# Kernel tuning notes

Measured on AMD Instinct MI355X. Metric: run time of the kernel, lower is better.

## Reference

```python
import jax, jax.numpy as jnp
import numpy as np

B, C, D_IN, D_H, D_OUT = 131072, 16, 256, 1024, 256


def setup_inputs() -> dict:
    key = jax.random.key(0)
    k = jax.random.split(key, 6)
    return {
        "x": jax.random.normal(k[0], (B, D_IN), dtype=jnp.float32),
        "cat_ids": jax.random.randint(k[1], (B,), 0, C, dtype=jnp.int32),
        "W1": jax.random.normal(k[2], (C, D_IN, D_H), dtype=jnp.float32) * (1.0 / np.sqrt(D_IN)),
        "b1": jax.random.normal(k[3], (C, D_H), dtype=jnp.float32) * 0.02,
        "W2": jax.random.normal(k[4], (C, D_H, D_OUT), dtype=jnp.float32) * (1.0 / np.sqrt(D_H)),
        "b2": jax.random.normal(k[5], (C, D_OUT), dtype=jnp.float32) * 0.02,
    }


def _routed_linear(x, cat_ids, W, b):
    # Category-routed linear: out[i] = x[i] @ W[cat_ids[i]] + b[cat_ids[i]].
    # Loop over the small fixed category count (not over tokens); each branch
    # is a dense GEMM masked by the routing assignment. This is equivalent to
    # the original gather -> per-category Linear -> scatter/argsort pattern
    # without materializing per-token weight gathers.
    num_categories = W.shape[0]
    out = jnp.zeros((x.shape[0], W.shape[2]), dtype=x.dtype)
    for c in range(num_categories):
        mask = (cat_ids == c)[:, None]
        out = out + jnp.where(mask, x @ W[c] + b[c], jnp.zeros((), x.dtype))
    return out


def reference(x, cat_ids, W1, b1, W2, b2):
    hidden = jax.nn.relu(_routed_linear(x, cat_ids, W1, b1))
    return _routed_linear(hidden, cat_ids, W2, b2)
```

## Files before the change

kernel.cpp:

```cpp
#include <hip/hip_runtime.h>
#include <hip/hip_bf16.h>

#define BB   131072
#define CC   16
#define DIN  256
#define DH   1024
#define DOUT 256
#define TM   64
#define NHB  32
#define NB   512

typedef __attribute__((ext_vector_type(8))) short bf16x8;
typedef __attribute__((ext_vector_type(4))) short short4v;
typedef __attribute__((ext_vector_type(4))) float f32x4;
typedef __attribute__((ext_vector_type(4))) float float4v;

__device__ inline unsigned short f2b(float f) {
  union { float f; unsigned u; } v; v.f = f;
  unsigned u = v.u;
  return (unsigned short)((u + 0x7fffu + ((u >> 16) & 1u)) >> 16);
}

__device__ inline void gload_lds16(const void* g, void* l) {
  __builtin_amdgcn_global_load_lds(
      (const __attribute__((address_space(1))) void*)g,
      (__attribute__((address_space(3))) void*)l, 16, 0, 0);
}

#define MFMA16(a, b, c) __builtin_amdgcn_mfma_f32_16x16x32_bf16((a), (b), (c), 0, 0, 0)

__global__ void hist_k(const int* __restrict__ cat, int* __restrict__ blockhist) {
  __shared__ int h[CC];
  const int tid = threadIdx.x;
  if (tid < CC) h[tid] = 0;
  __syncthreads();
  const int i = blockIdx.x * 256 + tid;
  atomicAdd(&h[cat[i]], 1);
  __syncthreads();
  if (tid < CC) blockhist[blockIdx.x * CC + tid] = h[tid];
}

__global__ void offsets2_k(const int* __restrict__ blockhist,
                           int* __restrict__ counts, int* __restrict__ padoff,
                           int* __restrict__ base) {
  __shared__ int part[CC][64];
  __shared__ int pref[CC][64];
  __shared__ int scnt[CC];
  __shared__ int spad[CC + 1];
  const int tid = threadIdx.x;
  const int c = tid >> 6;
  const int g = tid & 63;
  int h[8];
  int s = 0;
#pragma unroll
  for (int i = 0; i < 8; i++) {
    h[i] = blockhist[(g * 8 + i) * CC + c];
    s += h[i];
  }
  part[c][g] = s;
  __syncthreads();
  if (g == 0) {
    int r = 0;
    for (int j = 0; j < 64; j++) { pref[c][j] = r; r += part[c][j]; }
    scnt[c] = r;
  }
  __syncthreads();
  if (tid == 0) {
    int acc = 0;
    for (int c2 = 0; c2 < CC; c2++) {
      spad[c2] = acc;
      padoff[c2] = acc;
      counts[c2] = scnt[c2];
      acc += ((scnt[c2] + TM - 1) / TM) * TM;
    }
    spad[CC] = acc;
    padoff[CC] = acc;
  }
  __syncthreads();
  int run = spad[c] + pref[c][g];
#pragma unroll
  for (int i = 0; i < 8; i++) {
    base[(g * 8 + i) * CC + c] = run;
    run += h[i];
  }
}

__global__ void scatter2_k(const int* __restrict__ cat, const int* __restrict__ base,
                           int* __restrict__ idx) {
  __shared__ int cur[CC];
  const int tid = threadIdx.x;
  if (tid < CC) cur[tid] = base[blockIdx.x * CC + tid];
  __syncthreads();
  const int i = blockIdx.x * 256 + tid;
  const int c = cat[i];
  const int pos = atomicAdd(&cur[c], 1);
  idx[pos] = i;
}

__global__ void conv_w1_k(const float* __restrict__ W1, short* __restrict__ w1b) {
  int t = blockIdx.x * blockDim.x + threadIdx.x;
  int n  = t & 1023;
  int j8 = (t >> 10) & 31;
  int c  = t >> 15;
  const float* src = W1 + (size_t)c * DIN * DH;
  bf16x8 o;
#pragma unroll
  for (int i = 0; i < 8; i++)
    o[i] = (short)f2b(src[(size_t)(j8 * 8 + i) * DH + n]);
  char* dst = (char*)w1b + (size_t)c * 524288
            + (n >> 5) * 16384 + ((n >> 4) & 1) * 8192 + (j8 >> 2) * 1024
            + ((n & 15) + 16 * (j8 & 3)) * 16;
  *(bf16x8*)dst = o;
}

__global__ void conv_w2_k(const float* __restrict__ W2, short* __restrict__ w2b) {
  int t = blockIdx.x * blockDim.x + threadIdx.x;
  int n  = t & 255;
  int j8 = (t >> 8) & 127;
  int c  = t >> 15;
  const float* src = W2 + (size_t)c * DH * DOUT;
  bf16x8 o;
#pragma unroll
  for (int i = 0; i < 8; i++)
    o[i] = (short)f2b(src[(size_t)(j8 * 8 + i) * DOUT + n]);
  char* dst = (char*)w2b + (size_t)c * 524288
            + (j8 >> 2) * 16384 + (n >> 4) * 1024
            + ((n & 15) + 16 * (j8 & 3)) * 16;
  *(bf16x8*)dst = o;
}

#define W2OFF  32768
#define HSOFF  65536
#define TKOFF  69632
#define B1OFF  69888
#define B2OFF  73984
#define SMSZ   75008

__launch_bounds__(512, 4)
__global__ void mlp_k(const float* __restrict__ x,
                      const float* __restrict__ b1,
                      const float* __restrict__ b2,
                      const short* __restrict__ w1b,
                      const short* __restrict__ w2b,
                      const int* __restrict__ idx,
                      const int* __restrict__ padoff,
                      const int* __restrict__ counts,
                      float* __restrict__ out) {
  __shared__ __align__(16) char sm[SMSZ];

  const int bhw = blockIdx.x;
  const int wg = (bhw & 7) * 258 + (bhw >> 3);
  const int p = wg * TM;
  const int total = padoff[CC];
  if (p >= total) return;
  int c = 0;
  while (padoff[c + 1] <= p) c++;
  const int cnt = counts[c];
  const int start = p - padoff[c];

  const int tid  = threadIdx.x;
  const int lane = tid & 63;
  const int w    = tid >> 6;
  const int wt   = w >> 1;
  const int wh   = w & 1;
  const int lrow = lane & 15;
  const int lgrp = lane >> 4;

  char*  hsb   = sm + HSOFF;
  int*   toksp = (int*)(sm + TKOFF);
  float* b1s   = (float*)(sm + B1OFF);
  float* b2s   = (float*)(sm + B2OFF);

  {
    const int r = tid >> 3;
    const int q = tid & 7;
    const int pos = start + r;
    int tok = (pos < cnt) ? idx[p + r] : -1;
    if (q == 0) toksp[r] = tok;
    char* tilebase = sm + ((r >> 4) * 8 + q) * 1024 + (r & 15) * 16;
    if (tok >= 0) {
      const float4v* src = (const float4v*)(x + (size_t)tok * DIN) + q * 8;
#pragma unroll
      for (int m = 0; m < 4; m++) {
        float4v v0 = src[2 * m];
        float4v v1 = src[2 * m + 1];
        bf16x8 o;
        o[0] = (short)f2b(v0[0]); o[1] = (short)f2b(v0[1]);
        o[2] = (short)f2b(v0[2]); o[3] = (short)f2b(v0[3]);
        o[4] = (short)f2b(v1[0]); o[5] = (short)f2b(v1[1]);
        o[6] = (short)f2b(v1[2]); o[7] = (short)f2b(v1[3]);
        *(bf16x8*)(tilebase + m * 256) = o;
      }
    } else {
      bf16x8 z = {0, 0, 0, 0, 0, 0, 0, 0};
#pragma unroll
      for (int m = 0; m < 4; m++)
        *(bf16x8*)(tilebase + m * 256) = z;
    }
    if (tid < 256) ((f32x4*)b1s)[tid] = ((const f32x4*)(b1 + (size_t)c * DH))[tid];
    if (tid < 64)  ((f32x4*)b2s)[tid] = ((const f32x4*)(b2 + (size_t)c * DOUT))[tid];
  }
  __syncthreads();

  bf16x8 xf[8];
#pragma unroll
  for (int ks = 0; ks < 8; ks++)
    xf[ks] = *(const bf16x8*)(sm + (wt * 8 + ks) * 1024 + lane * 16);
  __syncthreads();

  const char* w1g = (const char*)w1b + (size_t)c * 524288;
  const char* w2g = (const char*)w2b + (size_t)c * 524288;

  auto stage1 = [&](int i) {
    const char* src = w1g + (size_t)i * 16384;
    char* dst = sm + (i & 1) * 16384;
#pragma unroll
    for (int j = 0; j < 2; j++) {
      int chunk = (w * 2 + j) * 1024;
      gload_lds16(src + chunk + lane * 16, dst + chunk);
    }
  };
  auto stage2 = [&](int i) {
    const char* src = w2g + (size_t)i * 16384;
    char* dst = sm + W2OFF + (i & 1) * 16384;
#pragma unroll
    for (int j = 0; j < 2; j++) {
      int chunk = (w * 2 + j) * 1024;
      gload_lds16(src + chunk + lane * 16, dst + chunk);
    }
  };

  stage1(0);
  stage2(0);
  asm volatile("s_waitcnt vmcnt(0)" ::: "memory");
  __syncthreads();

  f32x4 acc2[8];
#pragma unroll
  for (int ni = 0; ni < 8; ni++)
    acc2[ni] = (f32x4){0.f, 0.f, 0.f, 0.f};

  const int rtok = wt * 16 + lrow;
  char* hswr = hsb + wt * 1024 + (lrow + 16 * (wh * 2 + (lgrp >> 1))) * 16 + (lgrp & 1) * 8;

  for (int hb = 0; hb < NHB; hb++) {
    const char* w1c = sm + (hb & 1) * 16384 + wh * 8192;
    const char* w2c = sm + W2OFF + (hb & 1) * 16384 + wh * 8192;

    if (hb < NHB - 1) { stage1(hb + 1); stage2(hb + 1); }

    f32x4 acc1a = (f32x4){0.f, 0.f, 0.f, 0.f};
    f32x4 acc1b = (f32x4){0.f, 0.f, 0.f, 0.f};
#pragma unroll
    for (int ks = 0; ks < 8; ks += 2) {
      bf16x8 a0 = *(const bf16x8*)(w1c + ks * 1024 + lane * 16);
      bf16x8 a1 = *(const bf16x8*)(w1c + (ks + 1) * 1024 + lane * 16);
      acc1a = MFMA16(a0, xf[ks], acc1a);
      acc1b = MFMA16(a1, xf[ks + 1], acc1b);
    }
    {
      const int n0 = wh * 16 + lgrp * 4;
      f32x4 bv = *(const f32x4*)(b1s + hb * 32 + n0);
      short4v h;
#pragma unroll
      for (int jj = 0; jj < 4; jj++)
        h[jj] = (short)f2b(fmaxf(acc1a[jj] + acc1b[jj] + bv[jj], 0.0f));
      *(short4v*)hswr = h;
    }
    asm volatile("s_waitcnt vmcnt(4) lgkmcnt(0)" ::: "memory");
    __builtin_amdgcn_s_barrier();

    bf16x8 hf = *(const bf16x8*)(hsb + wt * 1024 + lane * 16);
#pragma unroll
    for (int ni = 0; ni < 8; ni++) {
      bf16x8 a2 = *(const bf16x8*)(w2c + ni * 1024 + lane * 16);
      acc2[ni] = MFMA16(a2, hf, acc2[ni]);
    }
    asm volatile("s_waitcnt vmcnt(2) lgkmcnt(0)" ::: "memory");
    __builtin_amdgcn_s_barrier();
  }

  const int tok = toksp[rtok];
  if (tok >= 0) {
#pragma unroll
    for (int ni = 0; ni < 8; ni++) {
      const int n0 = (wh * 8 + ni) * 16 + lgrp * 4;
      f32x4 bv = *(const f32x4*)(b2s + n0);
      f32x4 v = acc2[ni] + bv;
      *(f32x4*)(out + (size_t)tok * DOUT + n0) = v;
    }
  }
}

extern "C" void kernel_launch(void* const* d_in, const int* in_sizes, int n_in,
                              void* d_out, int out_size, void* d_ws, size_t ws_size,
                              hipStream_t stream) {
  (void)in_sizes; (void)n_in; (void)out_size; (void)ws_size;
  const float* x   = (const float*)d_in[0];
  const int*   cat = (const int*)d_in[1];
  const float* W1  = (const float*)d_in[2];
  const float* b1  = (const float*)d_in[3];
  const float* W2  = (const float*)d_in[4];
  const float* b2  = (const float*)d_in[5];
  float* out = (float*)d_out;

  char* ws = (char*)d_ws;
  int* counts    = (int*)(ws);
  int* padoff    = (int*)(ws + 128);
  int* blockhist = (int*)(ws + 4096);
  int* base      = (int*)(ws + 65536);
  int* idx       = (int*)(ws + 131072);
  short* w1b     = (short*)(ws + (1 << 20));
  short* w2b     = (short*)(ws + (1 << 20) + 8388608);

  hist_k<<<NB, 256, 0, stream>>>(cat, blockhist);
  offsets2_k<<<1, 1024, 0, stream>>>(blockhist, counts, padoff, base);
  scatter2_k<<<NB, 256, 0, stream>>>(cat, base, idx);
  conv_w1_k<<<2048, 256, 0, stream>>>(W1, w1b);
  conv_w2_k<<<2048, 256, 0, stream>>>(W2, w2b);

  const int ntiles = BB / TM + CC;
  mlp_k<<<ntiles, 512, 0, stream>>>(x, b1, b2, w1b, w2b, idx, padoff, counts, out);
}
```

Baseline: 236.6 us.

## Warp-specialize MLP kernel into producer/consumer waves with 128-row tiles

```diff
diff --git a/kernel.cpp b/kernel.cpp
--- a/kernel.cpp
+++ b/kernel.cpp
@@ -6,25 +6,18 @@
 #define DIN  256
 #define DH   1024
 #define DOUT 256
-#define TM   64
+#define TM   128
 #define NHB  32
 #define NB   512
 
 typedef __attribute__((ext_vector_type(8))) short bf16x8;
 typedef __attribute__((ext_vector_type(4))) short short4v;
 typedef __attribute__((ext_vector_type(4))) float f32x4;
-typedef __attribute__((ext_vector_type(4))) float float4v;
 
 __device__ inline unsigned short f2b(float f) {
   union { float f; unsigned u; } v; v.f = f;
   unsigned u = v.u;
   return (unsigned short)((u + 0x7fffu + ((u >> 16) & 1u)) >> 16);
-}
-
-__device__ inline void gload_lds16(const void* g, void* l) {
-  __builtin_amdgcn_global_load_lds(
-      (const __attribute__((address_space(1))) void*)g,
-      (__attribute__((address_space(3))) void*)l, 16, 0, 0);
 }
 
 #define MFMA16(a, b, c) __builtin_amdgcn_mfma_f32_16x16x32_bf16((a), (b), (c), 0, 0, 0)
@@ -129,14 +122,13 @@
   *(bf16x8*)dst = o;
 }
 
-#define W2OFF  32768
 #define HSOFF  65536
-#define TKOFF  69632
-#define B1OFF  69888
-#define B2OFF  73984
-#define SMSZ   75008
-
-__launch_bounds__(512, 4)
+#define TKOFF  81920
+#define B1OFF  82432
+#define B2OFF  86528
+#define SMSZ   87552
+
+__launch_bounds__(1024, 4)
 __global__ void mlp_k(const float* __restrict__ x,
                       const float* __restrict__ b1,
                       const float* __restrict__ b2,
@@ -149,7 +141,7 @@
   __shared__ __align__(16) char sm[SMSZ];
 
   const int bhw = blockIdx.x;
-  const int wg = (bhw & 7) * 258 + (bhw >> 3);
+  const int wg = (bhw & 7) * 130 + (bhw >> 3);
   const int p = wg * TM;
   const int total = padoff[CC];
   if (p >= total) return;
@@ -161,12 +153,10 @@
   const int tid  = threadIdx.x;
   const int lane = tid & 63;
   const int w    = tid >> 6;
-  const int wt   = w >> 1;
-  const int wh   = w & 1;
   const int lrow = lane & 15;
   const int lgrp = lane >> 4;
 
-  char*  hsb   = sm + HSOFF;
+  char*  hs0   = sm + HSOFF;
   int*   toksp = (int*)(sm + TKOFF);
   float* b1s   = (float*)(sm + B1OFF);
   float* b2s   = (float*)(sm + B2OFF);
@@ -179,11 +169,11 @@
     if (q == 0) toksp[r] = tok;
     char* tilebase = sm + ((r >> 4) * 8 + q) * 1024 + (r & 15) * 16;
     if (tok >= 0) {
-      const float4v* src = (const float4v*)(x + (size_t)tok * DIN) + q * 8;
+      const f32x4* src = (const f32x4*)(x + (size_t)tok * DIN) + q * 8;
 #pragma unroll
       for (int m = 0; m < 4; m++) {
-        float4v v0 = src[2 * m];
-        float4v v1 = src[2 * m + 1];
+        f32x4 v0 = src[2 * m];
+        f32x4 v1 = src[2 * m + 1];
         bf16x8 o;
         o[0] = (short)f2b(v0[0]); o[1] = (short)f2b(v0[1]);
         o[2] = (short)f2b(v0[2]); o[3] = (short)f2b(v0[3]);
@@ -202,92 +192,94 @@
   }
   __syncthreads();
 
-  bf16x8 xf[8];
-#pragma unroll
-  for (int ks = 0; ks < 8; ks++)
-    xf[ks] = *(const bf16x8*)(sm + (wt * 8 + ks) * 1024 + lane * 16);
-  __syncthreads();
+  const bool isprod = (w < 8);
+  const int tp = w & 3;
+  const int ph = (w >> 2) & 1;
+  const int cw = w & 7;
+  const int tq = cw & 1;
+  const int oq = cw >> 1;
+
+  bf16x8 xf[2][8];
+  if (isprod) {
+#pragma unroll
+    for (int t = 0; t < 2; t++)
+#pragma unroll
+      for (int ks = 0; ks < 8; ks++)
+        xf[t][ks] = *(const bf16x8*)(sm + (size_t)((2 * tp + t) * 8 + ks) * 1024 + lane * 16);
+  }
+
+  f32x4 acc2[4][4];
+  if (!isprod) {
+#pragma unroll
+    for (int j = 0; j < 4; j++)
+#pragma unroll
+      for (int i = 0; i < 4; i++)
+        acc2[j][i] = (f32x4){0.f, 0.f, 0.f, 0.f};
+  }
 
   const char* w1g = (const char*)w1b + (size_t)c * 524288;
   const char* w2g = (const char*)w2b + (size_t)c * 524288;
 
-  auto stage1 = [&](int i) {
-    const char* src = w1g + (size_t)i * 16384;
-    char* dst = sm + (i & 1) * 16384;
-#pragma unroll
-    for (int j = 0; j < 2; j++) {
-      int chunk = (w * 2 + j) * 1024;
-      gload_lds16(src + chunk + lane * 16, dst + chunk);
+  for (int hb = 0; hb <= NHB; hb++) {
+    if (isprod) {
+      if (hb < NHB) {
+        const char* w1p = w1g + hb * 16384 + ph * 8192;
+        f32x4 p0 = (f32x4){0.f, 0.f, 0.f, 0.f};
+        f32x4 p1 = (f32x4){0.f, 0.f, 0.f, 0.f};
+#pragma unroll
+        for (int ks = 0; ks < 8; ks++) {
+          bf16x8 a = *(const bf16x8*)(w1p + ks * 1024 + lane * 16);
+          p0 = MFMA16(a, xf[0][ks], p0);
+          p1 = MFMA16(a, xf[1][ks], p1);
+        }
+        f32x4 bv = *(const f32x4*)(b1s + hb * 32 + ph * 16 + lgrp * 4);
+        char* hw = hs0 + (hb & 1) * 8192
+                 + (lrow + 16 * (ph * 2 + (lgrp >> 1))) * 16 + (lgrp & 1) * 8;
+        short4v h0, h1;
+#pragma unroll
+        for (int jj = 0; jj < 4; jj++) {
+          h0[jj] = (short)f2b(fmaxf(p0[jj] + bv[jj], 0.0f));
+          h1[jj] = (short)f2b(fmaxf(p1[jj] + bv[jj], 0.0f));
+        }
+        *(short4v*)(hw + (2 * tp) * 1024)     = h0;
+        *(short4v*)(hw + (2 * tp + 1) * 1024) = h1;
+      }
+    } else {
+      if (hb > 0) {
+        const char* hr  = hs0 + ((hb - 1) & 1) * 8192;
+        const char* w2p = w2g + (size_t)(hb - 1) * 16384 + oq * 4096;
+        bf16x8 a2[4];
+#pragma unroll
+        for (int j = 0; j < 4; j++)
+          a2[j] = *(const bf16x8*)(w2p + j * 1024 + lane * 16);
+#pragma unroll
+        for (int i = 0; i < 4; i++) {
+          bf16x8 hf = *(const bf16x8*)(hr + (4 * tq + i) * 1024 + lane * 16);
+#pragma unroll
+          for (int j = 0; j < 4; j++)
+            acc2[j][i] = MFMA16(a2[j], hf, acc2[j][i]);
+        }
+      }
     }
-  };
-  auto stage2 = [&](int i) {
-    const char* src = w2g + (size_t)i * 16384;
-    char* dst = sm + W2OFF + (i & 1) * 16384;
-#pragma unroll
-    for (int j = 0; j < 2; j++) {
-      int chunk = (w * 2 + j) * 1024;
-      gload_lds16(src + chunk + lane * 16, dst + chunk);
-    }
-  };
-
-  stage1(0);
-  stage2(0);
-  asm volatile("s_waitcnt vmcnt(0)" ::: "memory");
-  __syncthreads();
-
-  f32x4 acc2[8];
-#pragma unroll
-  for (int ni = 0; ni < 8; ni++)
-    acc2[ni] = (f32x4){0.f, 0.f, 0.f, 0.f};
-
-  const int rtok = wt * 16 + lrow;
-  char* hswr = hsb + wt * 1024 + (lrow + 16 * (wh * 2 + (lgrp >> 1))) * 16 + (lgrp & 1) * 8;
-
-  for (int hb = 0; hb < NHB; hb++) {
-    const char* w1c = sm + (hb & 1) * 16384 + wh * 8192;
-    const char* w2c = sm + W2OFF + (hb & 1) * 16384 + wh * 8192;
-
-    if (hb < NHB - 1) { stage1(hb + 1); stage2(hb + 1); }
-
-    f32x4 acc1a = (f32x4){0.f, 0.f, 0.f, 0.f};
-    f32x4 acc1b = (f32x4){0.f, 0.f, 0.f, 0.f};
-#pragma unroll
-    for (int ks = 0; ks < 8; ks += 2) {
-      bf16x8 a0 = *(const bf16x8*)(w1c + ks * 1024 + lane * 16);
-      bf16x8 a1 = *(const bf16x8*)(w1c + (ks + 1) * 1024 + lane * 16);
-      acc1a = MFMA16(a0, xf[ks], acc1a);
-      acc1b = MFMA16(a1, xf[ks + 1], acc1b);
-    }
-    {
-      const int n0 = wh * 16 + lgrp * 4;
-      f32x4 bv = *(const f32x4*)(b1s + hb * 32 + n0);
-      short4v h;
-#pragma unroll
-      for (int jj = 0; jj < 4; jj++)
-        h[jj] = (short)f2b(fmaxf(acc1a[jj] + acc1b[jj] + bv[jj], 0.0f));
-      *(short4v*)hswr = h;
-    }
-    asm volatile("s_waitcnt vmcnt(4) lgkmcnt(0)" ::: "memory");
+    asm volatile("s_waitcnt lgkmcnt(0)" ::: "memory");
     __builtin_amdgcn_s_barrier();
-
-    bf16x8 hf = *(const bf16x8*)(hsb + wt * 1024 + lane * 16);
-#pragma unroll
-    for (int ni = 0; ni < 8; ni++) {
-      bf16x8 a2 = *(const bf16x8*)(w2c + ni * 1024 + lane * 16);
-      acc2[ni] = MFMA16(a2, hf, acc2[ni]);
-    }
-    asm volatile("s_waitcnt vmcnt(2) lgkmcnt(0)" ::: "memory");
-    __builtin_amdgcn_s_barrier();
-  }
-
-  const int tok = toksp[rtok];
-  if (tok >= 0) {
-#pragma unroll
-    for (int ni = 0; ni < 8; ni++) {
-      const int n0 = (wh * 8 + ni) * 16 + lgrp * 4;
-      f32x4 bv = *(const f32x4*)(b2s + n0);
-      f32x4 v = acc2[ni] + bv;
-      *(f32x4*)(out + (size_t)tok * DOUT + n0) = v;
+    __builtin_amdgcn_sched_barrier(0);
+  }
+
+  if (!isprod) {
+#pragma unroll
+    for (int i = 0; i < 4; i++) {
+      const int rr = (4 * tq + i) * 16 + lrow;
+      const int tok = toksp[rr];
+      if (tok >= 0) {
+#pragma unroll
+        for (int j = 0; j < 4; j++) {
+          const int n0 = (4 * oq + j) * 16 + lgrp * 4;
+          f32x4 bv = *(const f32x4*)(b2s + n0);
+          f32x4 v = acc2[j][i] + bv;
+          *(f32x4*)(out + (size_t)tok * DOUT + n0) = v;
+        }
+      }
     }
   }
 }
@@ -320,5 +312,5 @@
   conv_w2_k<<<2048, 256, 0, stream>>>(W2, w2b);
 
   const int ntiles = BB / TM + CC;
-  mlp_k<<<ntiles, 512, 0, stream>>>(x, b1, b2, w1b, w2b, idx, padoff, counts, out);
-}
+  mlp_k<<<ntiles, 1024, 0, stream>>>(x, b1, b2, w1b, w2b, idx, padoff, counts, out);
+}
```

Result: slower. 641.1 us (+171.0%).

## Double token tile to 128 rows so each wave reuses weight fragments

Applied to the files above, without the earlier changes.

```diff
diff --git a/kernel.cpp b/kernel.cpp
--- a/kernel.cpp
+++ b/kernel.cpp
@@ -6,14 +6,13 @@
 #define DIN  256
 #define DH   1024
 #define DOUT 256
-#define TM   64
-#define NHB  32
+#define TM   128
+#define NHB  16
 #define NB   512
 
 typedef __attribute__((ext_vector_type(8))) short bf16x8;
 typedef __attribute__((ext_vector_type(4))) short short4v;
 typedef __attribute__((ext_vector_type(4))) float f32x4;
-typedef __attribute__((ext_vector_type(4))) float float4v;
 
 __device__ inline unsigned short f2b(float f) {
   union { float f; unsigned u; } v; v.f = f;
@@ -108,7 +107,7 @@
   for (int i = 0; i < 8; i++)
     o[i] = (short)f2b(src[(size_t)(j8 * 8 + i) * DH + n]);
   char* dst = (char*)w1b + (size_t)c * 524288
-            + (n >> 5) * 16384 + ((n >> 4) & 1) * 8192 + (j8 >> 2) * 1024
+            + (n >> 6) * 32768 + ((n >> 4) & 3) * 8192 + (j8 >> 2) * 1024
             + ((n & 15) + 16 * (j8 & 3)) * 16;
   *(bf16x8*)dst = o;
 }
@@ -124,19 +123,19 @@
   for (int i = 0; i < 8; i++)
     o[i] = (short)f2b(src[(size_t)(j8 * 8 + i) * DOUT + n]);
   char* dst = (char*)w2b + (size_t)c * 524288
-            + (j8 >> 2) * 16384 + (n >> 4) * 1024
+            + (j8 >> 3) * 32768 + (n >> 4) * 2048 + ((j8 >> 2) & 1) * 1024
             + ((n & 15) + 16 * (j8 & 3)) * 16;
   *(bf16x8*)dst = o;
 }
 
-#define W2OFF  32768
-#define HSOFF  65536
-#define TKOFF  69632
-#define B1OFF  69888
-#define B2OFF  73984
-#define SMSZ   75008
-
-__launch_bounds__(512, 4)
+#define W2OFF  65536
+#define HSOFF  131072
+#define TKOFF  147456
+#define B1OFF  147968
+#define B2OFF  152064
+#define SMSZ   153088
+
+__launch_bounds__(512, 2)
 __global__ void mlp_k(const float* __restrict__ x,
                       const float* __restrict__ b1,
                       const float* __restrict__ b2,
@@ -149,7 +148,7 @@
   __shared__ __align__(16) char sm[SMSZ];
 
   const int bhw = blockIdx.x;
-  const int wg = (bhw & 7) * 258 + (bhw >> 3);
+  const int wg = (bhw & 7) * 130 + (bhw >> 3);
   const int p = wg * TM;
   const int total = padoff[CC];
   if (p >= total) return;
@@ -172,60 +171,62 @@
   float* b2s   = (float*)(sm + B2OFF);
 
   {
-    const int r = tid >> 3;
-    const int q = tid & 7;
+    const int r = tid >> 2;
+    const int q = tid & 3;
     const int pos = start + r;
     int tok = (pos < cnt) ? idx[p + r] : -1;
     if (q == 0) toksp[r] = tok;
-    char* tilebase = sm + ((r >> 4) * 8 + q) * 1024 + (r & 15) * 16;
+    char* tb = sm + (r >> 4) * 8192 + (r & 15) * 16;
     if (tok >= 0) {
-      const float4v* src = (const float4v*)(x + (size_t)tok * DIN) + q * 8;
-#pragma unroll
-      for (int m = 0; m < 4; m++) {
-        float4v v0 = src[2 * m];
-        float4v v1 = src[2 * m + 1];
+      const f32x4* src = (const f32x4*)(x + (size_t)tok * DIN) + q * 16;
+#pragma unroll
+      for (int t = 0; t < 8; t++) {
+        f32x4 v0 = src[2 * t];
+        f32x4 v1 = src[2 * t + 1];
         bf16x8 o;
         o[0] = (short)f2b(v0[0]); o[1] = (short)f2b(v0[1]);
         o[2] = (short)f2b(v0[2]); o[3] = (short)f2b(v0[3]);
         o[4] = (short)f2b(v1[0]); o[5] = (short)f2b(v1[1]);
         o[6] = (short)f2b(v1[2]); o[7] = (short)f2b(v1[3]);
-        *(bf16x8*)(tilebase + m * 256) = o;
+        *(bf16x8*)(tb + (2 * q + (t >> 2)) * 1024 + (t & 3) * 256) = o;
       }
     } else {
       bf16x8 z = {0, 0, 0, 0, 0, 0, 0, 0};
 #pragma unroll
-      for (int m = 0; m < 4; m++)
-        *(bf16x8*)(tilebase + m * 256) = z;
+      for (int t = 0; t < 8; t++)
+        *(bf16x8*)(tb + (2 * q + (t >> 2)) * 1024 + (t & 3) * 256) = z;
     }
     if (tid < 256) ((f32x4*)b1s)[tid] = ((const f32x4*)(b1 + (size_t)c * DH))[tid];
     if (tid < 64)  ((f32x4*)b2s)[tid] = ((const f32x4*)(b2 + (size_t)c * DOUT))[tid];
   }
   __syncthreads();
 
-  bf16x8 xf[8];
-#pragma unroll
-  for (int ks = 0; ks < 8; ks++)
-    xf[ks] = *(const bf16x8*)(sm + (wt * 8 + ks) * 1024 + lane * 16);
+  bf16x8 xf[2][8];
+#pragma unroll
+  for (int ti = 0; ti < 2; ti++)
+#pragma unroll
+    for (int ks = 0; ks < 8; ks++)
+      xf[ti][ks] = *(const bf16x8*)(sm + (2 * wt + ti) * 8192 + ks * 1024 + lane * 16);
   __syncthreads();
 
   const char* w1g = (const char*)w1b + (size_t)c * 524288;
   const char* w2g = (const char*)w2b + (size_t)c * 524288;
 
   auto stage1 = [&](int i) {
-    const char* src = w1g + (size_t)i * 16384;
-    char* dst = sm + (i & 1) * 16384;
-#pragma unroll
-    for (int j = 0; j < 2; j++) {
-      int chunk = (w * 2 + j) * 1024;
+    const char* src = w1g + (size_t)i * 32768;
+    char* dst = sm + (i & 1) * 32768;
+#pragma unroll
+    for (int j = 0; j < 4; j++) {
+      int chunk = (w * 4 + j) * 1024;
       gload_lds16(src + chunk + lane * 16, dst + chunk);
     }
   };
   auto stage2 = [&](int i) {
-    const char* src = w2g + (size_t)i * 16384;
-    char* dst = sm + W2OFF + (i & 1) * 16384;
-#pragma unroll
-    for (int j = 0; j < 2; j++) {
-      int chunk = (w * 2 + j) * 1024;
+    const char* src = w2g + (size_t)i * 32768;
+    char* dst = sm + W2OFF + (i & 1) * 32768;
+#pragma unroll
+    for (int j = 0; j < 4; j++) {
+      int chunk = (w * 4 + j) * 1024;
       gload_lds16(src + chunk + lane * 16, dst + chunk);
     }
   };
@@ -235,59 +236,81 @@
   asm volatile("s_waitcnt vmcnt(0)" ::: "memory");
   __syncthreads();
 
-  f32x4 acc2[8];
-#pragma unroll
-  for (int ni = 0; ni < 8; ni++)
-    acc2[ni] = (f32x4){0.f, 0.f, 0.f, 0.f};
-
-  const int rtok = wt * 16 + lrow;
-  char* hswr = hsb + wt * 1024 + (lrow + 16 * (wh * 2 + (lgrp >> 1))) * 16 + (lgrp & 1) * 8;
+  f32x4 acc2[2][8];
+#pragma unroll
+  for (int ti = 0; ti < 2; ti++)
+#pragma unroll
+    for (int ni = 0; ni < 8; ni++)
+      acc2[ti][ni] = (f32x4){0.f, 0.f, 0.f, 0.f};
 
   for (int hb = 0; hb < NHB; hb++) {
-    const char* w1c = sm + (hb & 1) * 16384 + wh * 8192;
-    const char* w2c = sm + W2OFF + (hb & 1) * 16384 + wh * 8192;
+    const char* w1c = sm + (hb & 1) * 32768;
+    const char* w2c = sm + W2OFF + (hb & 1) * 32768;
 
     if (hb < NHB - 1) { stage1(hb + 1); stage2(hb + 1); }
 
-    f32x4 acc1a = (f32x4){0.f, 0.f, 0.f, 0.f};
-    f32x4 acc1b = (f32x4){0.f, 0.f, 0.f, 0.f};
-#pragma unroll
-    for (int ks = 0; ks < 8; ks += 2) {
-      bf16x8 a0 = *(const bf16x8*)(w1c + ks * 1024 + lane * 16);
-      bf16x8 a1 = *(const bf16x8*)(w1c + (ks + 1) * 1024 + lane * 16);
-      acc1a = MFMA16(a0, xf[ks], acc1a);
-      acc1b = MFMA16(a1, xf[ks + 1], acc1b);
-    }
-    {
-      const int n0 = wh * 16 + lgrp * 4;
-      f32x4 bv = *(const f32x4*)(b1s + hb * 32 + n0);
-      short4v h;
-#pragma unroll
-      for (int jj = 0; jj < 4; jj++)
-        h[jj] = (short)f2b(fmaxf(acc1a[jj] + acc1b[jj] + bv[jj], 0.0f));
-      *(short4v*)hswr = h;
+    f32x4 acc1[2][2];
+#pragma unroll
+    for (int ti = 0; ti < 2; ti++)
+#pragma unroll
+      for (int nj = 0; nj < 2; nj++)
+        acc1[ti][nj] = (f32x4){0.f, 0.f, 0.f, 0.f};
+
+#pragma unroll
+    for (int ks = 0; ks < 8; ks++) {
+      bf16x8 a0 = *(const bf16x8*)(w1c + (2 * wh + 0) * 8192 + ks * 1024 + lane * 16);
+      bf16x8 a1 = *(const bf16x8*)(w1c + (2 * wh + 1) * 8192 + ks * 1024 + lane * 16);
+      acc1[0][0] = MFMA16(a0, xf[0][ks], acc1[0][0]);
+      acc1[1][0] = MFMA16(a0, xf[1][ks], acc1[1][0]);
+      acc1[0][1] = MFMA16(a1, xf[0][ks], acc1[0][1]);
+      acc1[1][1] = MFMA16(a1, xf[1][ks], acc1[1][1]);
+    }
+
+#pragma unroll
+    for (int nj = 0; nj < 2; nj++) {
+      f32x4 bv = *(const f32x4*)(b1s + hb * 64 + (2 * wh + nj) * 16 + lgrp * 4);
+#pragma unroll
+      for (int ti = 0; ti < 2; ti++) {
+        short4v h;
+#pragma unroll
+        for (int jj = 0; jj < 4; jj++)
+          h[jj] = (short)f2b(fmaxf(acc1[ti][nj][jj] + bv[jj], 0.0f));
+        *(short4v*)(hsb + (2 * wt + ti) * 2048 + wh * 1024
+                    + (lrow + 16 * (2 * nj + (lgrp >> 1))) * 16 + (lgrp & 1) * 8) = h;
+      }
+    }
+    if (hb < NHB - 1)
+      asm volatile("s_waitcnt vmcnt(8) lgkmcnt(0)" ::: "memory");
+    else
+      asm volatile("s_waitcnt vmcnt(0) lgkmcnt(0)" ::: "memory");
+    __builtin_amdgcn_s_barrier();
+
+#pragma unroll
+    for (int ks = 0; ks < 2; ks++) {
+      bf16x8 hf0 = *(const bf16x8*)(hsb + (2 * wt + 0) * 2048 + ks * 1024 + lane * 16);
+      bf16x8 hf1 = *(const bf16x8*)(hsb + (2 * wt + 1) * 2048 + ks * 1024 + lane * 16);
+#pragma unroll
+      for (int ni = 0; ni < 8; ni++) {
+        bf16x8 a2 = *(const bf16x8*)(w2c + (wh * 8 + ni) * 2048 + ks * 1024 + lane * 16);
+        acc2[0][ni] = MFMA16(a2, hf0, acc2[0][ni]);
+        acc2[1][ni] = MFMA16(a2, hf1, acc2[1][ni]);
+      }
     }
     asm volatile("s_waitcnt vmcnt(4) lgkmcnt(0)" ::: "memory");
     __builtin_amdgcn_s_barrier();
-
-    bf16x8 hf = *(const bf16x8*)(hsb + wt * 1024 + lane * 16);
-#pragma unroll
-    for (int ni = 0; ni < 8; ni++) {
-      bf16x8 a2 = *(const bf16x8*)(w2c + ni * 1024 + lane * 16);
-      acc2[ni] = MFMA16(a2, hf, acc2[ni]);
-    }
-    asm volatile("s_waitcnt vmcnt(2) lgkmcnt(0)" ::: "memory");
-    __builtin_amdgcn_s_barrier();
-  }
-
-  const int tok = toksp[rtok];
-  if (tok >= 0) {
-#pragma unroll
-    for (int ni = 0; ni < 8; ni++) {
-      const int n0 = (wh * 8 + ni) * 16 + lgrp * 4;
-      f32x4 bv = *(const f32x4*)(b2s + n0);
-      f32x4 v = acc2[ni] + bv;
-      *(f32x4*)(out + (size_t)tok * DOUT + n0) = v;
+  }
+
+#pragma unroll
+  for (int ti = 0; ti < 2; ti++) {
+    const int tok = toksp[(2 * wt + ti) * 16 + lrow];
+    if (tok >= 0) {
+#pragma unroll
+      for (int ni = 0; ni < 8; ni++) {
+        const int n0 = (wh * 8 + ni) * 16 + lgrp * 4;
+        f32x4 bv = *(const f32x4*)(b2s + n0);
+        f32x4 v = acc2[ti][ni] + bv;
+        *(f32x4*)(out + (size_t)tok * DOUT + n0) = v;
+      }
     }
   }
 }
```

Measured after the change: 243.8 us. 1.03x slower.

## Double token tile to 128 with 4 waves each owning two token subtiles

Applied to the files above, without the earlier changes.

```diff
diff --git a/kernel.cpp b/kernel.cpp
--- a/kernel.cpp
+++ b/kernel.cpp
@@ -6,14 +6,13 @@
 #define DIN  256
 #define DH   1024
 #define DOUT 256
-#define TM   64
+#define TM   128
 #define NHB  32
 #define NB   512
 
 typedef __attribute__((ext_vector_type(8))) short bf16x8;
 typedef __attribute__((ext_vector_type(4))) short short4v;
 typedef __attribute__((ext_vector_type(4))) float f32x4;
-typedef __attribute__((ext_vector_type(4))) float float4v;
 
 __device__ inline unsigned short f2b(float f) {
   union { float f; unsigned u; } v; v.f = f;
@@ -131,12 +130,12 @@
 
 #define W2OFF  32768
 #define HSOFF  65536
-#define TKOFF  69632
-#define B1OFF  69888
-#define B2OFF  73984
-#define SMSZ   75008
-
-__launch_bounds__(512, 4)
+#define TKOFF  73728
+#define B1OFF  74240
+#define B2OFF  78336
+#define SMSZ   79360
+
+__launch_bounds__(256, 2)
 __global__ void mlp_k(const float* __restrict__ x,
                       const float* __restrict__ b1,
                       const float* __restrict__ b2,
@@ -149,7 +148,7 @@
   __shared__ __align__(16) char sm[SMSZ];
 
   const int bhw = blockIdx.x;
-  const int wg = (bhw & 7) * 258 + (bhw >> 3);
+  const int wg = (bhw & 7) * 130 + (bhw >> 3);
   const int p = wg * TM;
   const int total = padoff[CC];
   if (p >= total) return;
@@ -161,51 +160,59 @@
   const int tid  = threadIdx.x;
   const int lane = tid & 63;
   const int w    = tid >> 6;
-  const int wt   = w >> 1;
-  const int wh   = w & 1;
   const int lrow = lane & 15;
   const int lgrp = lane >> 4;
 
-  char*  hsb   = sm + HSOFF;
+  char*  hsb   = sm + HSOFF + w * 2048;
   int*   toksp = (int*)(sm + TKOFF);
   float* b1s   = (float*)(sm + B1OFF);
   float* b2s   = (float*)(sm + B2OFF);
 
   {
-    const int r = tid >> 3;
-    const int q = tid & 7;
+    const int r = tid >> 1;
+    const int q = tid & 1;
     const int pos = start + r;
     int tok = (pos < cnt) ? idx[p + r] : -1;
     if (q == 0) toksp[r] = tok;
-    char* tilebase = sm + ((r >> 4) * 8 + q) * 1024 + (r & 15) * 16;
+    char* tb = sm + (r >> 4) * 8192 + (r & 15) * 16;
     if (tok >= 0) {
-      const float4v* src = (const float4v*)(x + (size_t)tok * DIN) + q * 8;
-#pragma unroll
-      for (int m = 0; m < 4; m++) {
-        float4v v0 = src[2 * m];
-        float4v v1 = src[2 * m + 1];
-        bf16x8 o;
-        o[0] = (short)f2b(v0[0]); o[1] = (short)f2b(v0[1]);
-        o[2] = (short)f2b(v0[2]); o[3] = (short)f2b(v0[3]);
-        o[4] = (short)f2b(v1[0]); o[5] = (short)f2b(v1[1]);
-        o[6] = (short)f2b(v1[2]); o[7] = (short)f2b(v1[3]);
-        *(bf16x8*)(tilebase + m * 256) = o;
+      const f32x4* src = (const f32x4*)(x + (size_t)tok * DIN);
+#pragma unroll
+      for (int k4 = 0; k4 < 4; k4++) {
+        const int ks = q * 4 + k4;
+#pragma unroll
+        for (int m = 0; m < 4; m++) {
+          f32x4 v0 = src[ks * 8 + m * 2];
+          f32x4 v1 = src[ks * 8 + m * 2 + 1];
+          bf16x8 o;
+          o[0] = (short)f2b(v0[0]); o[1] = (short)f2b(v0[1]);
+          o[2] = (short)f2b(v0[2]); o[3] = (short)f2b(v0[3]);
+          o[4] = (short)f2b(v1[0]); o[5] = (short)f2b(v1[1]);
+          o[6] = (short)f2b(v1[2]); o[7] = (short)f2b(v1[3]);
+          *(bf16x8*)(tb + ks * 1024 + 16 * (16 * m)) = o;
+        }
       }
     } else {
       bf16x8 z = {0, 0, 0, 0, 0, 0, 0, 0};
 #pragma unroll
-      for (int m = 0; m < 4; m++)
-        *(bf16x8*)(tilebase + m * 256) = z;
-    }
-    if (tid < 256) ((f32x4*)b1s)[tid] = ((const f32x4*)(b1 + (size_t)c * DH))[tid];
-    if (tid < 64)  ((f32x4*)b2s)[tid] = ((const f32x4*)(b2 + (size_t)c * DOUT))[tid];
-  }
-  __syncthreads();
-
-  bf16x8 xf[8];
-#pragma unroll
-  for (int ks = 0; ks < 8; ks++)
-    xf[ks] = *(const bf16x8*)(sm + (wt * 8 + ks) * 1024 + lane * 16);
+      for (int k4 = 0; k4 < 4; k4++) {
+        const int ks = q * 4 + k4;
+#pragma unroll
+        for (int m = 0; m < 4; m++)
+          *(bf16x8*)(tb + ks * 1024 + 16 * (16 * m)) = z;
+      }
+    }
+    ((f32x4*)b1s)[tid] = ((const f32x4*)(b1 + (size_t)c * DH))[tid];
+    if (tid < 64) ((f32x4*)b2s)[tid] = ((const f32x4*)(b2 + (size_t)c * DOUT))[tid];
+  }
+  __syncthreads();
+
+  bf16x8 xf[2][8];
+#pragma unroll
+  for (int ti = 0; ti < 2; ti++)
+#pragma unroll
+    for (int ks = 0; ks < 8; ks++)
+      xf[ti][ks] = *(const bf16x8*)(sm + (2 * w + ti) * 8192 + ks * 1024 + lane * 16);
   __syncthreads();
 
   const char* w1g = (const char*)w1b + (size_t)c * 524288;
@@ -215,8 +222,8 @@
     const char* src = w1g + (size_t)i * 16384;
     char* dst = sm + (i & 1) * 16384;
 #pragma unroll
-    for (int j = 0; j < 2; j++) {
-      int chunk = (w * 2 + j) * 1024;
+    for (int j = 0; j < 4; j++) {
+      int chunk = (w * 4 + j) * 1024;
       gload_lds16(src + chunk + lane * 16, dst + chunk);
     }
   };
@@ -224,8 +231,8 @@
     const char* src = w2g + (size_t)i * 16384;
     char* dst = sm + W2OFF + (i & 1) * 16384;
 #pragma unroll
-    for (int j = 0; j < 2; j++) {
-      int chunk = (w * 2 + j) * 1024;
+    for (int j = 0; j < 4; j++) {
+      int chunk = (w * 4 + j) * 1024;
       gload_lds16(src + chunk + lane * 16, dst + chunk);
     }
   };
@@ -235,59 +242,87 @@
   asm volatile("s_waitcnt vmcnt(0)" ::: "memory");
   __syncthreads();
 
-  f32x4 acc2[8];
-#pragma unroll
-  for (int ni = 0; ni < 8; ni++)
-    acc2[ni] = (f32x4){0.f, 0.f, 0.f, 0.f};
-
-  const int rtok = wt * 16 + lrow;
-  char* hswr = hsb + wt * 1024 + (lrow + 16 * (wh * 2 + (lgrp >> 1))) * 16 + (lgrp & 1) * 8;
-
-  for (int hb = 0; hb < NHB; hb++) {
-    const char* w1c = sm + (hb & 1) * 16384 + wh * 8192;
-    const char* w2c = sm + W2OFF + (hb & 1) * 16384 + wh * 8192;
-
-    if (hb < NHB - 1) { stage1(hb + 1); stage2(hb + 1); }
-
-    f32x4 acc1a = (f32x4){0.f, 0.f, 0.f, 0.f};
-    f32x4 acc1b = (f32x4){0.f, 0.f, 0.f, 0.f};
-#pragma unroll
-    for (int ks = 0; ks < 8; ks += 2) {
+  f32x4 acc2[2][16];
+#pragma unroll
+  for (int ti = 0; ti < 2; ti++)
+#pragma unroll
+    for (int ot = 0; ot < 16; ot++)
+      acc2[ti][ot] = (f32x4){0.f, 0.f, 0.f, 0.f};
+
+  const int hw0 = (lrow + 16 * (lgrp >> 1)) * 16 + (lgrp & 1) * 8;
+  const int hw1 = hw0 + 32 * 16;
+
+  for (int i = 0; i < NHB; i++) {
+    const char* w1c = sm + (i & 1) * 16384;
+    const char* w2c = sm + W2OFF + (i & 1) * 16384;
+    const bool notlast = (i < NHB - 1);
+
+    if (notlast) { stage1(i + 1); stage2(i + 1); }
+
+    f32x4 p00 = (f32x4){0.f, 0.f, 0.f, 0.f};
+    f32x4 p10 = (f32x4){0.f, 0.f, 0.f, 0.f};
+    f32x4 p01 = (f32x4){0.f, 0.f, 0.f, 0.f};
+    f32x4 p11 = (f32x4){0.f, 0.f, 0.f, 0.f};
+    __builtin_amdgcn_s_setprio(1);
+#pragma unroll
+    for (int ks = 0; ks < 8; ks++) {
       bf16x8 a0 = *(const bf16x8*)(w1c + ks * 1024 + lane * 16);
-      bf16x8 a1 = *(const bf16x8*)(w1c + (ks + 1) * 1024 + lane * 16);
-      acc1a = MFMA16(a0, xf[ks], acc1a);
-      acc1b = MFMA16(a1, xf[ks + 1], acc1b);
-    }
+      bf16x8 a1 = *(const bf16x8*)(w1c + 8192 + ks * 1024 + lane * 16);
+      p00 = MFMA16(a0, xf[0][ks], p00);
+      p10 = MFMA16(a0, xf[1][ks], p10);
+      p01 = MFMA16(a1, xf[0][ks], p01);
+      p11 = MFMA16(a1, xf[1][ks], p11);
+    }
+    __builtin_amdgcn_s_setprio(0);
+
     {
-      const int n0 = wh * 16 + lgrp * 4;
-      f32x4 bv = *(const f32x4*)(b1s + hb * 32 + n0);
+      f32x4 bv0 = *(const f32x4*)(b1s + i * 32 + lgrp * 4);
+      f32x4 bv1 = *(const f32x4*)(b1s + i * 32 + 16 + lgrp * 4);
       short4v h;
 #pragma unroll
-      for (int jj = 0; jj < 4; jj++)
-        h[jj] = (short)f2b(fmaxf(acc1a[jj] + acc1b[jj] + bv[jj], 0.0f));
-      *(short4v*)hswr = h;
-    }
-    asm volatile("s_waitcnt vmcnt(4) lgkmcnt(0)" ::: "memory");
-    __builtin_amdgcn_s_barrier();
-
-    bf16x8 hf = *(const bf16x8*)(hsb + wt * 1024 + lane * 16);
-#pragma unroll
-    for (int ni = 0; ni < 8; ni++) {
-      bf16x8 a2 = *(const bf16x8*)(w2c + ni * 1024 + lane * 16);
-      acc2[ni] = MFMA16(a2, hf, acc2[ni]);
-    }
-    asm volatile("s_waitcnt vmcnt(2) lgkmcnt(0)" ::: "memory");
-    __builtin_amdgcn_s_barrier();
-  }
-
-  const int tok = toksp[rtok];
-  if (tok >= 0) {
-#pragma unroll
-    for (int ni = 0; ni < 8; ni++) {
-      const int n0 = (wh * 8 + ni) * 16 + lgrp * 4;
-      f32x4 bv = *(const f32x4*)(b2s + n0);
-      f32x4 v = acc2[ni] + bv;
-      *(f32x4*)(out + (size_t)tok * DOUT + n0) = v;
+      for (int jj = 0; jj < 4; jj++) h[jj] = (short)f2b(fmaxf(p00[jj] + bv0[jj], 0.0f));
+      *(short4v*)(hsb + hw0) = h;
+#pragma unroll
+      for (int jj = 0; jj < 4; jj++) h[jj] = (short)f2b(fmaxf(p10[jj] + bv0[jj], 0.0f));
+      *(short4v*)(hsb + 1024 + hw0) = h;
+#pragma unroll
+      for (int jj = 0; jj < 4; jj++) h[jj] = (short)f2b(fmaxf(p01[jj] + bv1[jj], 0.0f));
+      *(short4v*)(hsb + hw1) = h;
+#pragma unroll
+      for (int jj = 0; jj < 4; jj++) h[jj] = (short)f2b(fmaxf(p11[jj] + bv1[jj], 0.0f));
+      *(short4v*)(hsb + 1024 + hw1) = h;
+    }
+
+    {
+      bf16x8 hf0 = *(const bf16x8*)(hsb + lane * 16);
+      bf16x8 hf1 = *(const bf16x8*)(hsb + 1024 + lane * 16);
+      __builtin_amdgcn_s_setprio(1);
+#pragma unroll
+      for (int ot = 0; ot < 16; ot++) {
+        bf16x8 a2 = *(const bf16x8*)(w2c + ot * 1024 + lane * 16);
+        acc2[0][ot] = MFMA16(a2, hf0, acc2[0][ot]);
+        acc2[1][ot] = MFMA16(a2, hf1, acc2[1][ot]);
+      }
+      __builtin_amdgcn_s_setprio(0);
+    }
+
+    if (notlast) {
+      asm volatile("s_waitcnt vmcnt(0)" ::: "memory");
+      __builtin_amdgcn_s_barrier();
+    }
+  }
+
+#pragma unroll
+  for (int ti = 0; ti < 2; ti++) {
+    const int tok = toksp[(2 * w + ti) * 16 + lrow];
+    if (tok >= 0) {
+#pragma unroll
+      for (int ot = 0; ot < 16; ot++) {
+        const int n0 = ot * 16 + lgrp * 4;
+        f32x4 bv = *(const f32x4*)(b2s + n0);
+        f32x4 v = acc2[ti][ot] + bv;
+        *(f32x4*)(out + (size_t)tok * DOUT + n0) = v;
+      }
     }
   }
 }
@@ -320,5 +355,5 @@
   conv_w2_k<<<2048, 256, 0, stream>>>(W2, w2b);
 
   const int ntiles = BB / TM + CC;
-  mlp_k<<<ntiles, 512, 0, stream>>>(x, b1, b2, w1b, w2b, idx, padoff, counts, out);
-}
+  mlp_k<<<ntiles, 256, 0, stream>>>(x, b1, b2, w1b, w2b, idx, padoff, counts, out);
+}
```

After: 353.0 us. 1.49x slower.
